# Kernel tuning notes

Hardware: AMD Instinct MI355X
Metric: run time of the kernel (lower is better)

## Reference

```python
import jax, jax.numpy as jnp
import numpy as np

N = 20000       # nodes
E = 320000      # edges
D_IN = 128
H = 512
OUT = 7
EPS = 1e-5


def setup_inputs() -> dict:
    key = jax.random.key(0)
    ks = jax.random.split(key, 16)
    def lin(k, fan_in, fan_out):
        bound = 1.0 / np.sqrt(fan_in)
        kw, kb = jax.random.split(k)
        W = jax.random.uniform(kw, (fan_in, fan_out), jnp.float32, -bound, bound)
        b = jax.random.uniform(kb, (fan_out,), jnp.float32, -bound, bound)
        return W, b
    x = jax.random.normal(ks[0], (N, D_IN), jnp.float32)
    edge_index = jax.random.randint(ks[1], (2, E), 0, N, dtype=jnp.int64)
    W1, b1 = lin(ks[2], D_IN, H)
    W2, b2 = lin(ks[3], H, H)
    W3, b3 = lin(ks[4], H, H)
    W4, b4 = lin(ks[5], H, H)
    ln_gamma = jnp.ones((H,), jnp.float32)
    ln_beta = jnp.zeros((H,), jnp.float32)
    W_out, b_out = lin(ks[6], H, OUT)
    return {"x": x, "edge_index": edge_index,
            "W1": W1, "b1": b1, "W2": W2, "b2": b2,
            "W3": W3, "b3": b3, "W4": W4, "b4": b4,
            "ln_gamma": ln_gamma, "ln_beta": ln_beta,
            "W_out": W_out, "b_out": b_out}


def _gcn_layer(x, W, b, src, dst, dinv):
    # transform, then symmetric-normalized gather/scatter-add (PyG GCNConv)
    h = x @ W                                    # [N, H]
    norm = dinv[src] * dinv[dst]                 # [E+N]
    msg = h[src] * norm[:, None]                 # gather + scale
    agg = jax.ops.segment_sum(msg, dst, num_segments=N)
    return agg + b


def reference(x, edge_index, W1, b1, W2, b2, W3, b3, W4, b4,
              ln_gamma, ln_beta, W_out, b_out):
    loops = jnp.arange(N, dtype=edge_index.dtype)
    src = jnp.concatenate([edge_index[0], loops])  # A + I self loops
    dst = jnp.concatenate([edge_index[1], loops])
    deg = jax.ops.segment_sum(jnp.ones_like(src, dtype=x.dtype), dst,
                              num_segments=N)
    dinv = jnp.where(deg > 0, jax.lax.rsqrt(deg), 0.0)

    def ln(h):
        mu = h.mean(-1, keepdims=True)
        var = h.var(-1, keepdims=True)
        return (h - mu) * jax.lax.rsqrt(var + EPS) * ln_gamma + ln_beta

    for W, b in ((W1, b1), (W2, b2), (W3, b3), (W4, b4)):
        x = jax.nn.relu(ln(_gcn_layer(x, W, b, src, dst, dinv)))
    g = x.mean(axis=0)           # mean pool over nodes -> [H]
    # dropout is identity in eval mode
    return g @ W_out + b_out     # [OUT]
```

## Files before the change

kernel.cpp:

```cpp
#include <hip/hip_runtime.h>

#define HID 512
#define OUTD 7
#define EPSV 1e-5f
#define PB 256
#define PR 32

typedef __attribute__((ext_vector_type(8))) short bf16x8;
typedef __attribute__((ext_vector_type(4))) float f32x4;
typedef __attribute__((ext_vector_type(2))) float f32x2;
typedef unsigned short ushort_t;
typedef unsigned int uint_t;
typedef unsigned char uchar_t;

__device__ __forceinline__ ushort_t f2bf(float f) {
    uint_t u = __float_as_uint(f);
    u = (u + 0x7fffu + ((u >> 16) & 1u)) >> 16;
    return (ushort_t)u;
}
__device__ __forceinline__ float bflo(uint_t u) { return __uint_as_float(u << 16); }
__device__ __forceinline__ float bfhi(uint_t u) { return __uint_as_float(u & 0xffff0000u); }

__device__ __forceinline__ void dec4(uint_t v, float* f) {
    f32x2 p0 = __builtin_amdgcn_cvt_pk_f32_fp8(v, false);
    f32x2 p1 = __builtin_amdgcn_cvt_pk_f32_fp8(v, true);
    f[0] = p0.x; f[1] = p0.y; f[2] = p1.x; f[3] = p1.y;
}
__device__ __forceinline__ uint_t enc4(float a, float b, float c, float d) {
    uint_t r = __builtin_amdgcn_cvt_pk_fp8_f32(a, b, 0, false);
    r = __builtin_amdgcn_cvt_pk_fp8_f32(c, d, r, true);
    return r;
}

__device__ __forceinline__ void gload_lds16(const ushort_t* g, ushort_t* l) {
    __builtin_amdgcn_global_load_lds(
        (const __attribute__((address_space(1))) uint_t*)g,
        (__attribute__((address_space(3))) uint_t*)l, 16, 0, 0);
}
__device__ __forceinline__ void gload_lds16_u8(const uchar_t* g, uchar_t* l) {
    __builtin_amdgcn_global_load_lds(
        (const __attribute__((address_space(1))) uint_t*)g,
        (__attribute__((address_space(3))) uint_t*)l, 16, 0, 0);
}


__global__ void deg_count(const int* __restrict__ dst, int* __restrict__ deg, int E) {
    int e = blockIdx.x * blockDim.x + threadIdx.x;
    if (e < E) atomicAdd(&deg[dst[e]], 1);
}

__global__ __launch_bounds__(256) void wtrans(
        const float* __restrict__ W0, const float* __restrict__ W1,
        const float* __restrict__ W2, const float* __restrict__ W3,
        ushort_t* __restrict__ T0, ushort_t* __restrict__ T1,
        ushort_t* __restrict__ T2, ushort_t* __restrict__ T3) {
    __shared__ ushort_t tile[32][33];
    int id = blockIdx.x;
    const float* W; ushort_t* T; int K;
    if (id < 64)       { W = W0; T = T0; K = 128; }
    else if (id < 320) { W = W1; T = T1; K = 512; id -= 64; }
    else if (id < 576) { W = W2; T = T2; K = 512; id -= 320; }
    else               { W = W3; T = T3; K = 512; id -= 576; }
    const int tn = id & 15;
    const int tk = id >> 4;
    const int t = threadIdx.x;
    const int r = t >> 3;
    const int c4 = (t & 7) * 4;
    const float4 v = *(const float4*)&W[(size_t)(tk * 32 + r) * HID + tn * 32 + c4];
    tile[r][c4 + 0] = f2bf(v.x); tile[r][c4 + 1] = f2bf(v.y);
    tile[r][c4 + 2] = f2bf(v.z); tile[r][c4 + 3] = f2bf(v.w);
    __syncthreads();
    ushort4 ov = make_ushort4(tile[c4 + 0][r], tile[c4 + 1][r],
                              tile[c4 + 2][r], tile[c4 + 3][r]);
    *(ushort4*)&T[(size_t)(tn * 32 + r) * K + tk * 32 + c4] = ov;
}


__global__ void scan1(const int* __restrict__ deg, int* __restrict__ off,
                      int* __restrict__ partial, float* __restrict__ dinv, int N) {
    __shared__ int s[256];
    const int t = threadIdx.x;
    const int i = blockIdx.x * 256 + t;
    int d = (i < N) ? deg[i] : 0;
    if (i < N) dinv[i] = rsqrtf((float)(d + 1));
    s[t] = d;
    __syncthreads();
#pragma unroll
    for (int ofs = 1; ofs < 256; ofs <<= 1) {
        int v = (t >= ofs) ? s[t - ofs] : 0;
        __syncthreads();
        s[t] += v;
        __syncthreads();
    }
    if (i < N) off[i] = s[t] - d;
    if (t == 255) partial[blockIdx.x] = s[255];
}

__global__ void scan23(int* __restrict__ off, const int* __restrict__ partial,
                       int* __restrict__ cursor, int N, int E, int nb) {
    __shared__ int s[256];
    __shared__ int ex[256];
    const int t = threadIdx.x;
    int d = (t < nb) ? partial[t] : 0;
    s[t] = d;
    __syncthreads();
#pragma unroll
    for (int ofs = 1; ofs < 256; ofs <<= 1) {
        int v = (t >= ofs) ? s[t - ofs] : 0;
        __syncthreads();
        s[t] += v;
        __syncthreads();
    }
    ex[t] = s[t] - d;
    __syncthreads();
    int i = blockIdx.x * 256 + t;
    if (i < N) {
        int v = off[i] + ex[i >> 8];
        off[i] = v;
        cursor[i] = v;
    } else if (i == N) {
        off[N] = E;
    }
}


__global__ void fill_cvt(const int* __restrict__ src, const int* __restrict__ dst,
                         int* __restrict__ cursor, int* __restrict__ srcs, int E,
                         const float* __restrict__ x, const float* __restrict__ dinv,
                         ushort_t* __restrict__ xb, int pairs) {
    int i = blockIdx.x * blockDim.x + threadIdx.x;
    if (i < E) { int p = atomicAdd(&cursor[dst[i]], 1); srcs[p] = src[i]; return; }
    i -= E;
    if (i < pairs) {
        float dr = dinv[i >> 6];
        float a = x[2 * i] * dr, b = x[2 * i + 1] * dr;
        uint_t d = __builtin_amdgcn_cvt_pk_fp8_f32(a, b, 0, false);
        xb[i] = (ushort_t)(d & 0xffffu);
    }
}


__global__ __launch_bounds__(256) void csr_agg_512(
        const uchar_t* __restrict__ xs, const int* __restrict__ off,
        const int* __restrict__ srcs, const float* __restrict__ dinv,
        uchar_t* __restrict__ ax, int N) {
    int gtid = blockIdx.x * 256 + threadIdx.x;
    int r = gtid >> 6, lane = gtid & 63;
    if (r >= N) return;
    const int half = lane >> 5, l32 = lane & 31;
    const uint4* xb = (const uint4*)xs;
    float a[16];
    if (half == 0) {
        uint4 v = xb[(size_t)r * 32 + l32];
        dec4(v.x, a); dec4(v.y, a + 4); dec4(v.z, a + 8); dec4(v.w, a + 12);
    } else {
#pragma unroll
        for (int q = 0; q < 16; q++) a[q] = 0.f;
    }
    int e = off[r];
    const int e1 = off[r + 1];
    for (; e + 8 <= e1; e += 8) {
        int si[4]; uint4 vi[4];
#pragma unroll
        for (int j = 0; j < 4; j++) si[j] = srcs[e + 2 * j + half];
#pragma unroll
        for (int j = 0; j < 4; j++) vi[j] = xb[(size_t)si[j] * 32 + l32];
#pragma unroll
        for (int j = 0; j < 4; j++) {
            float f[16];
            dec4(vi[j].x, f); dec4(vi[j].y, f + 4); dec4(vi[j].z, f + 8); dec4(vi[j].w, f + 12);
#pragma unroll
            for (int q = 0; q < 16; q++) a[q] += f[q];
        }
    }
    for (; e < e1; e += 2) {
        int idx = e + half;
        bool valid = idx < e1;
        int s = srcs[valid ? idx : e];
        uint4 v = xb[(size_t)s * 32 + l32];
        if (!valid) { v.x = 0; v.y = 0; v.z = 0; v.w = 0; }
        float f[16];
        dec4(v.x, f); dec4(v.y, f + 4); dec4(v.z, f + 8); dec4(v.w, f + 12);
#pragma unroll
        for (int q = 0; q < 16; q++) a[q] += f[q];
    }
#pragma unroll
    for (int q = 0; q < 16; q++) a[q] += __shfl_xor(a[q], 32);
    if (half == 0) {
        float dr = dinv[r];
        uint4 o;
        o.x = enc4(a[0] * dr,  a[1] * dr,  a[2] * dr,  a[3] * dr);
        o.y = enc4(a[4] * dr,  a[5] * dr,  a[6] * dr,  a[7] * dr);
        o.z = enc4(a[8] * dr,  a[9] * dr,  a[10] * dr, a[11] * dr);
        o.w = enc4(a[12] * dr, a[13] * dr, a[14] * dr, a[15] * dr);
        ((uint4*)ax)[(size_t)r * 32 + l32] = o;
    }
}

__global__ __launch_bounds__(256) void csr_agg_128(
        const uchar_t* __restrict__ xs, const int* __restrict__ off,
        const int* __restrict__ srcs, const float* __restrict__ dinv,
        uchar_t* __restrict__ ax, int N) {
    int gtid = blockIdx.x * 256 + threadIdx.x;
    int r = gtid >> 6, lane = gtid & 63;
    if (r >= N) return;
    const int sub = lane >> 3, l8 = lane & 7;
    const uint4* xb = (const uint4*)xs;
    float a[16];
    if (sub == 0) {
        uint4 v = xb[(size_t)r * 8 + l8];
        dec4(v.x, a); dec4(v.y, a + 4); dec4(v.z, a + 8); dec4(v.w, a + 12);
    } else {
#pragma unroll
        for (int q = 0; q < 16; q++) a[q] = 0.f;
    }
    const int e1 = off[r + 1];
    for (int e = off[r]; e < e1; e += 8) {
        int idx = e + sub;
        bool valid = idx < e1;
        int s = srcs[valid ? idx : e];
        uint4 v = xb[(size_t)s * 8 + l8];
        if (!valid) { v.x = 0; v.y = 0; v.z = 0; v.w = 0; }
        float f[16];
        dec4(v.x, f); dec4(v.y, f + 4); dec4(v.z, f + 8); dec4(v.w, f + 12);
#pragma unroll
        for (int q = 0; q < 16; q++) a[q] += f[q];
    }
#pragma unroll
    for (int q = 0; q < 16; q++) a[q] += __shfl_xor(a[q], 8);
#pragma unroll
    for (int q = 0; q < 16; q++) a[q] += __shfl_xor(a[q], 16);
#pragma unroll
    for (int q = 0; q < 16; q++) a[q] += __shfl_xor(a[q], 32);
    if (sub == 0) {
        float dr = dinv[r];
        uint4 o;
        o.x = enc4(a[0] * dr,  a[1] * dr,  a[2] * dr,  a[3] * dr);
        o.y = enc4(a[4] * dr,  a[5] * dr,  a[6] * dr,  a[7] * dr);
        o.z = enc4(a[8] * dr,  a[9] * dr,  a[10] * dr, a[11] * dr);
        o.w = enc4(a[12] * dr, a[13] * dr, a[14] * dr, a[15] * dr);
        ((uint4*)ax)[(size_t)r * 8 + l8] = o;
    }
}


__global__ __launch_bounds__(256) void gemm_mfma(
        const uchar_t* __restrict__ A, const ushort_t* __restrict__ Wt,
        const float* __restrict__ bias, ushort_t* __restrict__ C, int M, int K, int MB) {
    __shared__ __align__(16) uchar_t  As[4 * 128 * 16];
    __shared__ __align__(16) ushort_t Bs[8 * 128 * 8];
    const int id = blockIdx.x;
    const int mb = (id >> 5) * 8 + (id & 7);
    const int nbk = (id >> 3) & 3;
    if (mb >= MB) return;
    const int t = threadIdx.x;
    const int wave = t >> 6, lane = t & 63;
    const int m0 = mb * 128, n0 = nbk * 128;
    const int wm = (wave & 1) * 64, wn = (wave >> 1) * 64;
    const int quad = lane >> 4, l16 = lane & 15;

    f32x4 acc[4][4];
#pragma unroll
    for (int i = 0; i < 4; i++)
#pragma unroll
        for (int j = 0; j < 4; j++) acc[i][j] = (f32x4){0.f, 0.f, 0.f, 0.f};

    for (int k0 = 0; k0 < K; k0 += 64) {
#pragma unroll
        for (int h = 0; h < 2; h++) {
            int gm = m0 + 64 * h + lane;
            if (gm >= M) gm = M - 1;
            gload_lds16_u8(A + (size_t)gm * K + k0 + wave * 16,
                           &As[(wave * 128 + 64 * h) * 16]);
        }
#pragma unroll
        for (int h = 0; h < 4; h++) {
            int cb = wave * 2 + (h >> 1);
            int row = (h & 1) * 64 + lane;
            gload_lds16(Wt + (size_t)(n0 + row) * K + k0 + cb * 8,
                        &Bs[(cb * 128 + (h & 1) * 64) * 8]);
        }
        __syncthreads();
#pragma unroll
        for (int kk = 0; kk < 2; kk++) {
            bf16x8 af[4], bfr[4];
#pragma unroll
            for (int jn = 0; jn < 4; jn++)
                bfr[jn] = *(const bf16x8*)&Bs[((kk * 4 + quad) * 128 + wn + jn * 16 + l16) * 8];
#pragma unroll
            for (int i = 0; i < 4; i++) {
                uint2 v8 = *(const uint2*)&As[((kk * 2 + (quad >> 1)) * 128 + wm + i * 16 + l16) * 16
                                              + (quad & 1) * 8];
                f32x2 p0 = __builtin_amdgcn_cvt_pk_f32_fp8(v8.x, false);
                f32x2 p1 = __builtin_amdgcn_cvt_pk_f32_fp8(v8.x, true);
                f32x2 p2 = __builtin_amdgcn_cvt_pk_f32_fp8(v8.y, false);
                f32x2 p3 = __builtin_amdgcn_cvt_pk_f32_fp8(v8.y, true);
                union { uint_t u[4]; bf16x8 v; } pk;
                pk.u[0] = (__float_as_uint(p0.y) & 0xffff0000u) | (__float_as_uint(p0.x) >> 16);
                pk.u[1] = (__float_as_uint(p1.y) & 0xffff0000u) | (__float_as_uint(p1.x) >> 16);
                pk.u[2] = (__float_as_uint(p2.y) & 0xffff0000u) | (__float_as_uint(p2.x) >> 16);
                pk.u[3] = (__float_as_uint(p3.y) & 0xffff0000u) | (__float_as_uint(p3.x) >> 16);
                af[i] = pk.v;
            }
#pragma unroll
            for (int i = 0; i < 4; i++)
#pragma unroll
                for (int jn = 0; jn < 4; jn++)
                    acc[i][jn] = __builtin_amdgcn_mfma_f32_16x16x32_bf16(
                                     af[i], bfr[jn], acc[i][jn], 0, 0, 0);
        }
        __syncthreads();
    }
#pragma unroll
    for (int i = 0; i < 4; i++) {
#pragma unroll
        for (int jn = 0; jn < 4; jn++) {
            int gn = n0 + wn + jn * 16 + l16;
            float bv = bias[gn];
#pragma unroll
            for (int rg = 0; rg < 4; rg++) {
                int gm = m0 + wm + i * 16 + quad * 4 + rg;
                if (gm < M) C[(size_t)gm * HID + gn] = f2bf(acc[i][jn][rg] + bv);
            }
        }
    }
}


__global__ void ln_relu(const ushort_t* __restrict__ h, const float* __restrict__ gamma,
                        const float* __restrict__ beta, const float* __restrict__ dinv,
                        void* __restrict__ optr, int N) {
    int gtid = blockIdx.x * blockDim.x + threadIdx.x;
    int r = gtid >> 6, lane = gtid & 63;
    if (r >= N) return;
    uint4 v = ((const uint4*)(h + (size_t)r * HID))[lane];
    float f[8] = {bflo(v.x), bfhi(v.x), bflo(v.y), bfhi(v.y),
                  bflo(v.z), bfhi(v.z), bflo(v.w), bfhi(v.w)};
    float s = 0.f, q = 0.f;
#pragma unroll
    for (int j = 0; j < 8; j++) { s += f[j]; q += f[j] * f[j]; }
#pragma unroll
    for (int ofs = 32; ofs > 0; ofs >>= 1) {
        s += __shfl_xor(s, ofs);
        q += __shfl_xor(q, ofs);
    }
    float mu  = s * (1.0f / HID);
    float var = q * (1.0f / HID) - mu * mu;
    float rs  = rsqrtf(var + EPSV);
    float dr  = dinv[r];
    const float4* gp = (const float4*)gamma;
    const float4* bp = (const float4*)beta;
    float4 g0 = gp[2 * lane], g1 = gp[2 * lane + 1];
    float4 b0 = bp[2 * lane], b1 = bp[2 * lane + 1];
    float gg[8] = {g0.x, g0.y, g0.z, g0.w, g1.x, g1.y, g1.z, g1.w};
    float bb[8] = {b0.x, b0.y, b0.z, b0.w, b1.x, b1.y, b1.z, b1.w};
    float o[8];
#pragma unroll
    for (int j = 0; j < 8; j++)
        o[j] = fmaxf((f[j] - mu) * rs * gg[j] + bb[j], 0.f) * dr;
    uint2 ov;
    ov.x = enc4(o[0], o[1], o[2], o[3]);
    ov.y = enc4(o[4], o[5], o[6], o[7]);
    ((uint2*)optr)[(size_t)r * 64 + lane] = ov;
}


__global__ __launch_bounds__(256) void ln_pool(
        const ushort_t* __restrict__ h, const float* __restrict__ gamma,
        const float* __restrict__ beta, float* __restrict__ pbuf, int N) {
    __shared__ float sred[4][64][8];
    const int t = threadIdx.x;
    const int sub = t >> 6, lane = t & 63;
    const float4* gp = (const float4*)gamma;
    const float4* bp = (const float4*)beta;
    float4 g0 = gp[2 * lane], g1 = gp[2 * lane + 1];
    float4 b0 = bp[2 * lane], b1 = bp[2 * lane + 1];
    float gg[8] = {g0.x, g0.y, g0.z, g0.w, g1.x, g1.y, g1.z, g1.w};
    float bb[8] = {b0.x, b0.y, b0.z, b0.w, b1.x, b1.y, b1.z, b1.w};
    float colacc[8] = {0.f, 0.f, 0.f, 0.f, 0.f, 0.f, 0.f, 0.f};
    const int step = PB * 4;
    for (int r = blockIdx.x * 4 + sub; r < N; r += step) {
        uint4 v = ((const uint4*)(h + (size_t)r * HID))[lane];
        float f[8] = {bflo(v.x), bfhi(v.x), bflo(v.y), bfhi(v.y),
                      bflo(v.z), bfhi(v.z), bflo(v.w), bfhi(v.w)};
        float s = 0.f, q = 0.f;
#pragma unroll
        for (int j = 0; j < 8; j++) { s += f[j]; q += f[j] * f[j]; }
#pragma unroll
        for (int ofs = 32; ofs > 0; ofs >>= 1) {
            s += __shfl_xor(s, ofs);
            q += __shfl_xor(q, ofs);
        }
        float mu  = s * (1.0f / HID);
        float var = q * (1.0f / HID) - mu * mu;
        float rs  = rsqrtf(var + EPSV);
#pragma unroll
        for (int j = 0; j < 8; j++)
            colacc[j] += fmaxf((f[j] - mu) * rs * gg[j] + bb[j], 0.f);
    }
#pragma unroll
    for (int j = 0; j < 8; j++) sred[sub][lane][j] = colacc[j];
    __syncthreads();
    if (sub == 0) {
        float4 o0, o1;
        o0.x = sred[0][lane][0] + sred[1][lane][0] + sred[2][lane][0] + sred[3][lane][0];
        o0.y = sred[0][lane][1] + sred[1][lane][1] + sred[2][lane][1] + sred[3][lane][1];
        o0.z = sred[0][lane][2] + sred[1][lane][2] + sred[2][lane][2] + sred[3][lane][2];
        o0.w = sred[0][lane][3] + sred[1][lane][3] + sred[2][lane][3] + sred[3][lane][3];
        o1.x = sred[0][lane][4] + sred[1][lane][4] + sred[2][lane][4] + sred[3][lane][4];
        o1.y = sred[0][lane][5] + sred[1][lane][5] + sred[2][lane][5] + sred[3][lane][5];
        o1.z = sred[0][lane][6] + sred[1][lane][6] + sred[2][lane][6] + sred[3][lane][6];
        o1.w = sred[0][lane][7] + sred[1][lane][7] + sred[2][lane][7] + sred[3][lane][7];
        float* pb = pbuf + (size_t)blockIdx.x * HID + lane * 8;
        ((float4*)pb)[0] = o0;
        ((float4*)pb)[1] = o1;
    }
}


__global__ __launch_bounds__(256) void pool_reduce(
        const float* __restrict__ pbuf, float* __restrict__ pbuf2) {
    const int t = threadIdx.x;
    const int b = blockIdx.x;
    const int R = PB / PR;
    float2 s = make_float2(0.f, 0.f);
#pragma unroll
    for (int u = 0; u < R; u++) {
        const float2 v = ((const float2*)(pbuf + (size_t)(b * R + u) * HID))[t];
        s.x += v.x; s.y += v.y;
    }
    ((float2*)(pbuf2 + (size_t)b * HID))[t] = s;
}


__global__ void out_kernel(const float* __restrict__ pbuf2, const float* __restrict__ Wout,
                           const float* __restrict__ bout, float* __restrict__ out, int N) {
    __shared__ float red[256];
    int t = threadIdx.x;
    float g0 = 0.f, g1 = 0.f;
#pragma unroll
    for (int p = 0; p < PR; p += 8) {
#pragma unroll
        for (int u = 0; u < 8; u++) {
            const float2 v = ((const float2*)(pbuf2 + (size_t)(p + u) * HID))[t];
            g0 += v.x; g1 += v.y;
        }
    }
    float invn = 1.0f / (float)N;
    for (int o = 0; o < OUTD; o++) {
        float pr = g0 * Wout[(2 * t) * OUTD + o] + g1 * Wout[(2 * t + 1) * OUTD + o];
        red[t] = pr;
        __syncthreads();
        for (int sft = 128; sft > 0; sft >>= 1) {
            if (t < sft) red[t] += red[t + sft];
            __syncthreads();
        }
        if (t == 0) out[o] = red[0] * invn + bout[o];
        __syncthreads();
    }
}


extern "C" void kernel_launch(void* const* d_in, const int* in_sizes, int n_in,
                              void* d_out, int out_size, void* d_ws, size_t ws_size,
                              hipStream_t stream) {
    const float* x  = (const float*)d_in[0];
    const int*   ei = (const int*)d_in[1];
    const int N = in_sizes[0] / 128;
    const int E = in_sizes[1] / 2;
    const int* src = ei;
    const int* dst = ei + E;
    const float* Ws[4] = {(const float*)d_in[2], (const float*)d_in[4],
                          (const float*)d_in[6], (const float*)d_in[8]};
    const float* bs[4] = {(const float*)d_in[3], (const float*)d_in[5],
                          (const float*)d_in[7], (const float*)d_in[9]};
    const float* gamma = (const float*)d_in[10];
    const float* beta  = (const float*)d_in[11];
    const float* Wout  = (const float*)d_in[12];
    const float* bout  = (const float*)d_in[13];
    float* out = (float*)d_out;

    char* p = (char*)d_ws;
    uchar_t*  axb = (uchar_t*)p;   p += (size_t)N * HID;
    ushort_t* hb  = (ushort_t*)p;  p += sizeof(ushort_t) * (size_t)N * HID;
    uchar_t*  ho8 = (uchar_t*)p;   p += (size_t)N * HID;
    uchar_t*  xb8 = ho8;
    ushort_t* Wt[4];
    Wt[0] = (ushort_t*)p;          p += sizeof(ushort_t) * 128 * HID;
    Wt[1] = (ushort_t*)p;          p += sizeof(ushort_t) * HID * HID;
    Wt[2] = (ushort_t*)p;          p += sizeof(ushort_t) * HID * HID;
    Wt[3] = (ushort_t*)p;          p += sizeof(ushort_t) * HID * HID;
    float* dinv  = (float*)p;      p += sizeof(float) * N;
    float* pbuf  = (float*)p;      p += sizeof(float) * PB * HID;
    float* pbuf2 = (float*)p;      p += sizeof(float) * PR * HID;
    int* deg    = (int*)p;         p += sizeof(int) * N;
    int* off    = (int*)p;         p += sizeof(int) * (N + 4);
    int* cursor = (int*)p;         p += sizeof(int) * N;
    int* partial= (int*)p;         p += sizeof(int) * 256;
    int* srcs   = (int*)p;

    const int nb = (N + 255) / 256;
    const int MB = (N + 127) / 128;
    const int gemm_blocks = 32 * ((MB + 7) / 8);

    hipMemsetAsync(deg, 0, sizeof(int) * N, stream);
    deg_count<<<(E + 255) / 256, 256, 0, stream>>>(dst, deg, E);
    wtrans<<<832, 256, 0, stream>>>(Ws[0], Ws[1], Ws[2], Ws[3],
                                    Wt[0], Wt[1], Wt[2], Wt[3]);
    scan1<<<nb, 256, 0, stream>>>(deg, off, partial, dinv, N);
    scan23<<<(N + 256) / 256, 256, 0, stream>>>(off, partial, cursor, N, E, nb);
    {
        int pairs = N * 64;
        int tot = E + pairs;
        fill_cvt<<<(tot + 255) / 256, 256, 0, stream>>>(src, dst, cursor, srcs, E,
                                                        x, dinv, (ushort_t*)xb8, pairs);
    }

    for (int l = 0; l < 4; l++) {
        const int K = (l == 0) ? 128 : HID;
        if (l == 0)
            csr_agg_128<<<(N * 64 + 255) / 256, 256, 0, stream>>>(xb8, off, srcs, dinv, axb, N);
        else
            csr_agg_512<<<(N * 64 + 255) / 256, 256, 0, stream>>>(ho8, off, srcs, dinv, axb, N);
        gemm_mfma<<<gemm_blocks, 256, 0, stream>>>(axb, Wt[l], bs[l], hb, N, K, MB);
        if (l < 3)
            ln_relu<<<(N * 64 + 255) / 256, 256, 0, stream>>>(hb, gamma, beta, dinv, ho8, N);
        else
            ln_pool<<<PB, 256, 0, stream>>>(hb, gamma, beta, pbuf, N);
    }
    pool_reduce<<<PR, 256, 0, stream>>>(pbuf, pbuf2);
    out_kernel<<<1, 256, 0, stream>>>(pbuf2, Wout, bout, out, N);
}
```

Measured before the change: 373.1 us.

## Store aggregated activations as bf16 and use swizzled bf16 LDS tiles in GEMM

The aggregation kernels now write their normalized output as bf16 instead of fp8. The GEMM therefore loads A directly as bf16 into an XOR-swizzled LDS layout, with no per-fragment fp8-to-bf16 decode, and B uses the same swizzle. The degree-count and weight-transpose kernels are merged into one launch. This removes conversion ALU work and a launch, and gains accuracy, at the cost of twice the traffic for the aggregated activation buffer.

```diff
diff --git a/kernel.cpp b/kernel.cpp
--- a/kernel.cpp
+++ b/kernel.cpp
@@ -37,25 +37,20 @@
         (const __attribute__((address_space(1))) uint_t*)g,
         (__attribute__((address_space(3))) uint_t*)l, 16, 0, 0);
 }
-__device__ __forceinline__ void gload_lds16_u8(const uchar_t* g, uchar_t* l) {
-    __builtin_amdgcn_global_load_lds(
-        (const __attribute__((address_space(1))) uint_t*)g,
-        (__attribute__((address_space(3))) uint_t*)l, 16, 0, 0);
-}
-
-
-__global__ void deg_count(const int* __restrict__ dst, int* __restrict__ deg, int E) {
-    int e = blockIdx.x * blockDim.x + threadIdx.x;
-    if (e < E) atomicAdd(&deg[dst[e]], 1);
-}
-
-__global__ __launch_bounds__(256) void wtrans(
+
+__global__ __launch_bounds__(256) void deg_wtrans(
+        const int* __restrict__ dst, int* __restrict__ deg, int E, int degB,
         const float* __restrict__ W0, const float* __restrict__ W1,
         const float* __restrict__ W2, const float* __restrict__ W3,
         ushort_t* __restrict__ T0, ushort_t* __restrict__ T1,
         ushort_t* __restrict__ T2, ushort_t* __restrict__ T3) {
     __shared__ ushort_t tile[32][33];
-    int id = blockIdx.x;
+    if ((int)blockIdx.x < degB) {
+        int e = blockIdx.x * 256 + threadIdx.x;
+        if (e < E) atomicAdd(&deg[dst[e]], 1);
+        return;
+    }
+    int id = blockIdx.x - degB;
     const float* W; ushort_t* T; int K;
     if (id < 64)       { W = W0; T = T0; K = 128; }
     else if (id < 320) { W = W1; T = T1; K = 512; id -= 64; }
@@ -143,7 +138,7 @@
 __global__ __launch_bounds__(256) void csr_agg_512(
         const uchar_t* __restrict__ xs, const int* __restrict__ off,
         const int* __restrict__ srcs, const float* __restrict__ dinv,
-        uchar_t* __restrict__ ax, int N) {
+        ushort_t* __restrict__ ax, int N) {
     int gtid = blockIdx.x * 256 + threadIdx.x;
     int r = gtid >> 6, lane = gtid & 63;
     if (r >= N) return;
@@ -186,21 +181,21 @@
     }
 #pragma unroll
     for (int q = 0; q < 16; q++) a[q] += __shfl_xor(a[q], 32);
-    if (half == 0) {
+    {
         float dr = dinv[r];
-        uint4 o;
-        o.x = enc4(a[0] * dr,  a[1] * dr,  a[2] * dr,  a[3] * dr);
-        o.y = enc4(a[4] * dr,  a[5] * dr,  a[6] * dr,  a[7] * dr);
-        o.z = enc4(a[8] * dr,  a[9] * dr,  a[10] * dr, a[11] * dr);
-        o.w = enc4(a[12] * dr, a[13] * dr, a[14] * dr, a[15] * dr);
-        ((uint4*)ax)[(size_t)r * 32 + l32] = o;
+        const int b = half * 8;
+        uint_t w0 = (uint_t)f2bf(a[b + 0] * dr) | ((uint_t)f2bf(a[b + 1] * dr) << 16);
+        uint_t w1 = (uint_t)f2bf(a[b + 2] * dr) | ((uint_t)f2bf(a[b + 3] * dr) << 16);
+        uint_t w2 = (uint_t)f2bf(a[b + 4] * dr) | ((uint_t)f2bf(a[b + 5] * dr) << 16);
+        uint_t w3 = (uint_t)f2bf(a[b + 6] * dr) | ((uint_t)f2bf(a[b + 7] * dr) << 16);
+        ((uint4*)ax)[(size_t)r * 64 + l32 * 2 + half] = make_uint4(w0, w1, w2, w3);
     }
 }
 
 __global__ __launch_bounds__(256) void csr_agg_128(
         const uchar_t* __restrict__ xs, const int* __restrict__ off,
         const int* __restrict__ srcs, const float* __restrict__ dinv,
-        uchar_t* __restrict__ ax, int N) {
+        ushort_t* __restrict__ ax, int N) {
     int gtid = blockIdx.x * 256 + threadIdx.x;
     int r = gtid >> 6, lane = gtid & 63;
     if (r >= N) return;
@@ -232,23 +227,23 @@
     for (int q = 0; q < 16; q++) a[q] += __shfl_xor(a[q], 16);
 #pragma unroll
     for (int q = 0; q < 16; q++) a[q] += __shfl_xor(a[q], 32);
-    if (sub == 0) {
+    if (sub < 2) {
         float dr = dinv[r];
-        uint4 o;
-        o.x = enc4(a[0] * dr,  a[1] * dr,  a[2] * dr,  a[3] * dr);
-        o.y = enc4(a[4] * dr,  a[5] * dr,  a[6] * dr,  a[7] * dr);
-        o.z = enc4(a[8] * dr,  a[9] * dr,  a[10] * dr, a[11] * dr);
-        o.w = enc4(a[12] * dr, a[13] * dr, a[14] * dr, a[15] * dr);
-        ((uint4*)ax)[(size_t)r * 8 + l8] = o;
+        const int b = sub * 8;
+        uint_t w0 = (uint_t)f2bf(a[b + 0] * dr) | ((uint_t)f2bf(a[b + 1] * dr) << 16);
+        uint_t w1 = (uint_t)f2bf(a[b + 2] * dr) | ((uint_t)f2bf(a[b + 3] * dr) << 16);
+        uint_t w2 = (uint_t)f2bf(a[b + 4] * dr) | ((uint_t)f2bf(a[b + 5] * dr) << 16);
+        uint_t w3 = (uint_t)f2bf(a[b + 6] * dr) | ((uint_t)f2bf(a[b + 7] * dr) << 16);
+        ((uint4*)ax)[(size_t)r * 16 + l8 * 2 + sub] = make_uint4(w0, w1, w2, w3);
     }
 }
 
 
 __global__ __launch_bounds__(256) void gemm_mfma(
-        const uchar_t* __restrict__ A, const ushort_t* __restrict__ Wt,
+        const ushort_t* __restrict__ A, const ushort_t* __restrict__ Wt,
         const float* __restrict__ bias, ushort_t* __restrict__ C, int M, int K, int MB) {
-    __shared__ __align__(16) uchar_t  As[4 * 128 * 16];
-    __shared__ __align__(16) ushort_t Bs[8 * 128 * 8];
+    __shared__ __align__(16) ushort_t AsL[128 * 64];
+    __shared__ __align__(16) ushort_t BsL[128 * 64];
     const int id = blockIdx.x;
     const int mb = (id >> 5) * 8 + (id & 7);
     const int nbk = (id >> 3) & 3;
@@ -258,6 +253,9 @@
     const int m0 = mb * 128, n0 = nbk * 128;
     const int wm = (wave & 1) * 64, wn = (wave >> 1) * 64;
     const int quad = lane >> 4, l16 = lane & 15;
+    const int srow = lane >> 3;
+    const int schunk = (lane & 7) ^ srow;
+    const int sw = (l16 & 7) << 4;
 
     f32x4 acc[4][4];
 #pragma unroll
@@ -267,41 +265,27 @@
 
     for (int k0 = 0; k0 < K; k0 += 64) {
 #pragma unroll
-        for (int h = 0; h < 2; h++) {
-            int gm = m0 + 64 * h + lane;
+        for (int j = 0; j < 4; j++) {
+            const int c = wave * 4 + j;
+            int gm = m0 + 8 * c + srow;
             if (gm >= M) gm = M - 1;
-            gload_lds16_u8(A + (size_t)gm * K + k0 + wave * 16,
-                           &As[(wave * 128 + 64 * h) * 16]);
-        }
-#pragma unroll
-        for (int h = 0; h < 4; h++) {
-            int cb = wave * 2 + (h >> 1);
-            int row = (h & 1) * 64 + lane;
-            gload_lds16(Wt + (size_t)(n0 + row) * K + k0 + cb * 8,
-                        &Bs[(cb * 128 + (h & 1) * 64) * 8]);
+            gload_lds16(A + (size_t)gm * K + k0 + (schunk << 3), AsL + c * 512);
+            gload_lds16(Wt + (size_t)(n0 + 8 * c + srow) * K + k0 + (schunk << 3),
+                        BsL + c * 512);
         }
         __syncthreads();
 #pragma unroll
         for (int kk = 0; kk < 2; kk++) {
+            const int kb = (kk * 4 + quad) << 4;
             bf16x8 af[4], bfr[4];
 #pragma unroll
             for (int jn = 0; jn < 4; jn++)
-                bfr[jn] = *(const bf16x8*)&Bs[((kk * 4 + quad) * 128 + wn + jn * 16 + l16) * 8];
-#pragma unroll
-            for (int i = 0; i < 4; i++) {
-                uint2 v8 = *(const uint2*)&As[((kk * 2 + (quad >> 1)) * 128 + wm + i * 16 + l16) * 16
-                                              + (quad & 1) * 8];
-                f32x2 p0 = __builtin_amdgcn_cvt_pk_f32_fp8(v8.x, false);
-                f32x2 p1 = __builtin_amdgcn_cvt_pk_f32_fp8(v8.x, true);
-                f32x2 p2 = __builtin_amdgcn_cvt_pk_f32_fp8(v8.y, false);
-                f32x2 p3 = __builtin_amdgcn_cvt_pk_f32_fp8(v8.y, true);
-                union { uint_t u[4]; bf16x8 v; } pk;
-                pk.u[0] = (__float_as_uint(p0.y) & 0xffff0000u) | (__float_as_uint(p0.x) >> 16);
-                pk.u[1] = (__float_as_uint(p1.y) & 0xffff0000u) | (__float_as_uint(p1.x) >> 16);
-                pk.u[2] = (__float_as_uint(p2.y) & 0xffff0000u) | (__float_as_uint(p2.x) >> 16);
-                pk.u[3] = (__float_as_uint(p3.y) & 0xffff0000u) | (__float_as_uint(p3.x) >> 16);
-                af[i] = pk.v;
-            }
+                bfr[jn] = *(const bf16x8*)((const char*)BsL
+                              + (wn + jn * 16 + l16) * 128 + (kb ^ sw));
+#pragma unroll
+            for (int i = 0; i < 4; i++)
+                af[i] = *(const bf16x8*)((const char*)AsL
+                              + (wm + i * 16 + l16) * 128 + (kb ^ sw));
 #pragma unroll
             for (int i = 0; i < 4; i++)
 #pragma unroll
@@ -481,7 +465,7 @@
     float* out = (float*)d_out;
 
     char* p = (char*)d_ws;
-    uchar_t*  axb = (uchar_t*)p;   p += (size_t)N * HID;
+    ushort_t* axb = (ushort_t*)p;  p += sizeof(ushort_t) * (size_t)N * HID;
     ushort_t* hb  = (ushort_t*)p;  p += sizeof(ushort_t) * (size_t)N * HID;
     uchar_t*  ho8 = (uchar_t*)p;   p += (size_t)N * HID;
     uchar_t*  xb8 = ho8;
@@ -502,11 +486,12 @@
     const int nb = (N + 255) / 256;
     const int MB = (N + 127) / 128;
     const int gemm_blocks = 32 * ((MB + 7) / 8);
+    const int degB = (E + 255) / 256;
 
     hipMemsetAsync(deg, 0, sizeof(int) * N, stream);
-    deg_count<<<(E + 255) / 256, 256, 0, stream>>>(dst, deg, E);
-    wtrans<<<832, 256, 0, stream>>>(Ws[0], Ws[1], Ws[2], Ws[3],
-                                    Wt[0], Wt[1], Wt[2], Wt[3]);
+    deg_wtrans<<<degB + 832, 256, 0, stream>>>(dst, deg, E, degB,
+                                               Ws[0], Ws[1], Ws[2], Ws[3],
+                                               Wt[0], Wt[1], Wt[2], Wt[3]);
     scan1<<<nb, 256, 0, stream>>>(deg, off, partial, dinv, N);
     scan23<<<(N + 256) / 256, 256, 0, stream>>>(off, partial, cursor, N, E, nb);
     {
```

Measured after the change: 362.1 us. 1.03x faster.
